# Kernel tuning notes

Hardware: AMD Instinct MI355X
Metric: run time of the kernel (lower is better)

## Reference

```python
import math
import jax, jax.numpy as jnp
import numpy as np

# --- module constants (from init_kwargs) ---
N_PIX = 1024
NV = 64
PIX_SCALE = 0.1            # arcsec / pixel
SIGMA_PIX = 0.8
TRUNCATE = 3.0
FOV_HALF = 0.5 * (N_PIX - 1) * PIX_SCALE


def setup_inputs() -> dict:
    key = jax.random.key(0)
    k1, k2, k3 = jax.random.split(key, 3)
    n_clouds, k_vel = 200_000, 8
    # positions uniform inside the field of view (slightly inset)
    pos_img = (jax.random.uniform(k1, (n_clouds, k_vel, 2), dtype=jnp.float32) * 2.0 - 1.0) * (FOV_HALF * 0.95)
    # uniform velocity axis and in-range cloud velocities
    vel_axis = (-400.0 + 12.5 * jnp.arange(NV, dtype=jnp.float32))
    vel_chan = jax.random.uniform(k2, (n_clouds, k_vel), dtype=jnp.float32) * 780.0 - 395.0
    flux = jax.random.uniform(k3, (n_clouds, k_vel), dtype=jnp.float32)
    # normalized separable Gaussian kernel, truncated at TRUNCATE sigma
    half = int(math.ceil(TRUNCATE * SIGMA_PIX))
    x = jnp.arange(-half, half + 1, dtype=jnp.float32)
    g1d = jnp.exp(-0.5 * (x / SIGMA_PIX) ** 2)
    g1d = g1d / g1d.sum()
    kernel2d = (g1d[:, None] * g1d[None, :])[None, None]  # (1,1,7,7)
    return {"pos_img": pos_img, "vel_chan": vel_chan, "flux": flux,
            "vel_axis": vel_axis, "kernel2d": kernel2d}


def reference(pos_img, vel_chan, flux, vel_axis, kernel2d):
    Nv = vel_axis.shape[0]
    vel0 = vel_axis[0]
    dv = vel_axis[1] - vel_axis[0]

    ra = pos_img[..., 0].reshape(-1)   # (M,)
    dec = pos_img[..., 1].reshape(-1)
    vel = vel_chan.reshape(-1)
    flx = flux.reshape(-1)

    # nearest (floor) voxel index per point; fractional parts are unused
    ix0 = jnp.floor((ra + FOV_HALF) / PIX_SCALE).astype(jnp.int32)
    iy0 = jnp.floor((dec + FOV_HALF) / PIX_SCALE).astype(jnp.int32)
    iv0 = jnp.floor((vel - vel0) / dv).astype(jnp.int32)

    margin = kernel2d.shape[-1] // 2 + 1
    mask = ((ix0 >= -margin) & (ix0 < N_PIX + margin)
            & (iy0 >= -margin) & (iy0 < N_PIX + margin)
            & (iv0 >= 0) & (iv0 < Nv))
    flx = jnp.where(mask, flx, 0.0)

    # scatter-add fluxes into flattened cube (out-of-range indices dropped)
    idx_flat = (iv0 * N_PIX + iy0) * N_PIX + ix0
    cube = (jnp.zeros(Nv * N_PIX * N_PIX, dtype=flx.dtype)
            .at[idx_flat].add(flx, mode="drop")
            .reshape(Nv, N_PIX, N_PIX))

    # 'same' 2D Gaussian convolution per velocity channel
    out = jax.lax.conv_general_dilated(cube[:, None, :, :], kernel2d,
                                       window_strides=(1, 1), padding="SAME")
    return out[:, 0]
```

## Files before the change

kernel.cpp:

```cpp
#include <hip/hip_runtime.h>
#include <math.h>

#define N_PIX 1024
#define NV 64
#define NT 16
#define TILE 64
#define HALO 70
#define CAP 320
#define NBINS (NV * NT * NT)
#define CUBE_ELEMS (NV * N_PIX * N_PIX)
#define RS 72
#define HS 68

__global__ __launch_bounds__(256) void splat_bin(
    const float2* __restrict__ pos,
    const float*  __restrict__ vel_chan,
    const float*  __restrict__ flux,
    const float*  __restrict__ vel_axis,
    unsigned*     __restrict__ cnt,
    uint2*        __restrict__ entries, int M)
{
    int i = blockIdx.x * 256 + threadIdx.x;
    if (i >= M) return;

    const float FOV_HALF = 51.15f;
    const float INV_PIX  = 10.0f;
    const float vel0 = vel_axis[0];
    const float dv   = vel_axis[1] - vel0;

    float2 p = pos[i];
    float  v = vel_chan[i];
    float  f = flux[i];

    int ix0 = (int)floorf((p.x + FOV_HALF) * INV_PIX);
    int iy0 = (int)floorf((p.y + FOV_HALF) * INV_PIX);
    int iv0 = (int)floorf((v - vel0) / dv);

    const int margin = 4;
    if (!(ix0 >= -margin && ix0 < N_PIX + margin &&
          iy0 >= -margin && iy0 < N_PIX + margin &&
          iv0 >= 0 && iv0 < NV)) return;

    int idx = (iv0 * N_PIX + iy0) * N_PIX + ix0;
    if (idx < 0 || idx >= CUBE_ELEMS) return;
    int iv = idx >> 20;
    int iy = (idx >> 10) & 1023;
    int ix = idx & 1023;

    int tx = ix >> 6, ty = iy >> 6;
    int fx = ix & 63, fy = iy & 63;

    #pragma unroll
    for (int dy = -1; dy <= 1; ++dy) {
        if (dy < 0 && (fy >= 3 || ty == 0)) continue;
        if (dy > 0 && (fy < 61 || ty == NT - 1)) continue;
        int ly  = fy + 3 - 64 * dy;
        int byb = (iv * NT + (ty + dy)) * NT;
        #pragma unroll
        for (int dx = -1; dx <= 1; ++dx) {
            if (dx < 0 && (fx >= 3 || tx == 0)) continue;
            if (dx > 0 && (fx < 61 || tx == NT - 1)) continue;
            int lx  = fx + 3 - 64 * dx;
            int bin = byb + tx + dx;
            unsigned pos_ = atomicAdd(&cnt[bin], 1u);
            if (pos_ < CAP)
                entries[(size_t)bin * CAP + pos_] =
                    make_uint2((unsigned)((ly << 7) | lx), __float_as_uint(f));
        }
    }
}

__global__ __launch_bounds__(256) void conv_tile(
    const unsigned* __restrict__ cnt,
    const uint2*    __restrict__ entries,
    const float*    __restrict__ k2d,
    float*          __restrict__ out)
{
    __shared__ float raw[HALO * RS];
    __shared__ float hb [HALO * HS];

    const int t   = threadIdx.x;
    const int ch  = blockIdx.y;
    const int bin = ch * (NT * NT) + blockIdx.x;

    float g[7];
    {
        float g3 = sqrtf(k2d[24]);
        #pragma unroll
        for (int j = 0; j < 7; ++j) g[j] = k2d[21 + j] / g3;
    }

    for (int i4 = t; i4 < HALO * RS / 4; i4 += 256)
        ((float4*)raw)[i4] = make_float4(0.f, 0.f, 0.f, 0.f);
    __syncthreads();

    unsigned n = cnt[bin];
    if (n > CAP) n = CAP;
    const uint2* e = entries + (size_t)bin * CAP;
    for (unsigned i = t; i < n; i += 256) {
        uint2 u = e[i];
        atomicAdd(&raw[(u.x >> 7) * RS + (u.x & 127)], __uint_as_float(u.y));
    }
    __syncthreads();

    for (int p = t; p < HALO * 16; p += 256) {
        int r  = p >> 4;
        int xg = (p & 15) << 2;
        const float* rp = &raw[r * RS + xg];
        float4 a = *(const float4*)(rp);
        float4 b = *(const float4*)(rp + 4);
        float4 c = *(const float4*)(rp + 8);
        float rr[12] = {a.x, a.y, a.z, a.w, b.x, b.y, b.z, b.w, c.x, c.y, c.z, c.w};
        float s0 = 0.f, s1 = 0.f, s2 = 0.f, s3 = 0.f;
        #pragma unroll
        for (int j = 0; j < 7; ++j) {
            s0 = fmaf(rr[j],     g[j], s0);
            s1 = fmaf(rr[j + 1], g[j], s1);
            s2 = fmaf(rr[j + 2], g[j], s2);
            s3 = fmaf(rr[j + 3], g[j], s3);
        }
        *(float4*)&hb[r * HS + xg] = make_float4(s0, s1, s2, s3);
    }
    __syncthreads();

    const int xg   = (t & 15) << 2;
    const int rblk = t >> 4;
    const int q0   = rblk * 4;

    float4 w[8];
    #pragma unroll
    for (int j = 0; j < 6; ++j)
        w[j] = *(const float4*)&hb[(q0 + j) * HS + xg];

    const int ty = blockIdx.x >> 4, tx = blockIdx.x & 15;
    float* __restrict__ dst = out + ((size_t)ch << 20);
    const int row0 = ty * TILE + q0;
    const int colb = tx * TILE + xg;

    #pragma unroll
    for (int i = 0; i < 4; ++i) {
        w[(i + 6) & 7] = *(const float4*)&hb[(q0 + i + 6) * HS + xg];
        float4 acc = make_float4(0.f, 0.f, 0.f, 0.f);
        #pragma unroll
        for (int k = 0; k < 7; ++k) {
            float4 h4 = w[(i + k) & 7];
            acc.x = fmaf(h4.x, g[k], acc.x);
            acc.y = fmaf(h4.y, g[k], acc.y);
            acc.z = fmaf(h4.z, g[k], acc.z);
            acc.w = fmaf(h4.w, g[k], acc.w);
        }
        *(float4*)(dst + ((size_t)(row0 + i) << 10) + colb) = acc;
    }
}

extern "C" void kernel_launch(void* const* d_in, const int* in_sizes, int n_in,
                              void* d_out, int out_size, void* d_ws, size_t ws_size,
                              hipStream_t stream)
{
    const float2* pos      = (const float2*)d_in[0];
    const float*  vel_chan = (const float*)d_in[1];
    const float*  flux     = (const float*)d_in[2];
    const float*  vel_axis = (const float*)d_in[3];
    const float*  k2d      = (const float*)d_in[4];
    float* out = (float*)d_out;

    unsigned* cnt     = (unsigned*)d_ws;
    uint2*    entries = (uint2*)((char*)d_ws + (1 << 20));

    const int M = in_sizes[1];

    hipMemsetAsync(cnt, 0, NBINS * sizeof(unsigned), stream);

    splat_bin<<<(M + 255) / 256, 256, 0, stream>>>(
        pos, vel_chan, flux, vel_axis, cnt, entries, M);

    conv_tile<<<dim3(NT * NT, NV), 256, 0, stream>>>(cnt, entries, k2d, out);
}
```

Before: 422.8 us.

## Fuse horizontal and vertical blur passes in registers; use nontemporal output stores

Each thread now computes the horizontal pass for the ten rows it needs directly into registers, then applies the vertical pass. This removes the intermediate shared-memory buffer and one barrier. The raw row stride changes to 76 floats, and the output is written with nontemporal stores so the large result cube streams past the cache. In exchange, horizontal work is recomputed (10 rows per 4 output rows instead of about 70/64), and register pressure goes up.

```diff
diff --git a/kernel.cpp b/kernel.cpp
--- a/kernel.cpp
+++ b/kernel.cpp
@@ -9,8 +9,9 @@
 #define CAP 320
 #define NBINS (NV * NT * NT)
 #define CUBE_ELEMS (NV * N_PIX * N_PIX)
-#define RS 72
-#define HS 68
+#define RS 76
+
+typedef float f32x4 __attribute__((ext_vector_type(4)));
 
 __global__ __launch_bounds__(256) void splat_bin(
     const float2* __restrict__ pos,
@@ -77,7 +78,6 @@
     float*          __restrict__ out)
 {
     __shared__ float raw[HALO * RS];
-    __shared__ float hb [HALO * HS];
 
     const int t   = threadIdx.x;
     const int ch  = blockIdx.y;
@@ -103,53 +103,43 @@
     }
     __syncthreads();
 
-    for (int p = t; p < HALO * 16; p += 256) {
-        int r  = p >> 4;
-        int xg = (p & 15) << 2;
-        const float* rp = &raw[r * RS + xg];
+    const int xg = (t & 15) << 2;
+    const int q0 = (t >> 4) << 2;
+
+    float4 h[10];
+    #pragma unroll
+    for (int j = 0; j < 10; ++j) {
+        const float* rp = &raw[(q0 + j) * RS + xg];
         float4 a = *(const float4*)(rp);
         float4 b = *(const float4*)(rp + 4);
         float4 c = *(const float4*)(rp + 8);
         float rr[12] = {a.x, a.y, a.z, a.w, b.x, b.y, b.z, b.w, c.x, c.y, c.z, c.w};
         float s0 = 0.f, s1 = 0.f, s2 = 0.f, s3 = 0.f;
         #pragma unroll
-        for (int j = 0; j < 7; ++j) {
-            s0 = fmaf(rr[j],     g[j], s0);
-            s1 = fmaf(rr[j + 1], g[j], s1);
-            s2 = fmaf(rr[j + 2], g[j], s2);
-            s3 = fmaf(rr[j + 3], g[j], s3);
+        for (int jj = 0; jj < 7; ++jj) {
+            s0 = fmaf(rr[jj],     g[jj], s0);
+            s1 = fmaf(rr[jj + 1], g[jj], s1);
+            s2 = fmaf(rr[jj + 2], g[jj], s2);
+            s3 = fmaf(rr[jj + 3], g[jj], s3);
         }
-        *(float4*)&hb[r * HS + xg] = make_float4(s0, s1, s2, s3);
+        h[j] = make_float4(s0, s1, s2, s3);
     }
-    __syncthreads();
-
-    const int xg   = (t & 15) << 2;
-    const int rblk = t >> 4;
-    const int q0   = rblk * 4;
-
-    float4 w[8];
-    #pragma unroll
-    for (int j = 0; j < 6; ++j)
-        w[j] = *(const float4*)&hb[(q0 + j) * HS + xg];
 
     const int ty = blockIdx.x >> 4, tx = blockIdx.x & 15;
-    float* __restrict__ dst = out + ((size_t)ch << 20);
-    const int row0 = ty * TILE + q0;
-    const int colb = tx * TILE + xg;
-
+    float* __restrict__ dst = out + ((size_t)ch << 20)
+                            + ((size_t)(ty * TILE + q0) << 10) + tx * TILE + xg;
     #pragma unroll
     for (int i = 0; i < 4; ++i) {
-        w[(i + 6) & 7] = *(const float4*)&hb[(q0 + i + 6) * HS + xg];
         float4 acc = make_float4(0.f, 0.f, 0.f, 0.f);
         #pragma unroll
         for (int k = 0; k < 7; ++k) {
-            float4 h4 = w[(i + k) & 7];
-            acc.x = fmaf(h4.x, g[k], acc.x);
-            acc.y = fmaf(h4.y, g[k], acc.y);
-            acc.z = fmaf(h4.z, g[k], acc.z);
-            acc.w = fmaf(h4.w, g[k], acc.w);
+            acc.x = fmaf(h[i + k].x, g[k], acc.x);
+            acc.y = fmaf(h[i + k].y, g[k], acc.y);
+            acc.z = fmaf(h[i + k].z, g[k], acc.z);
+            acc.w = fmaf(h[i + k].w, g[k], acc.w);
         }
-        *(float4*)(dst + ((size_t)(row0 + i) << 10) + colb) = acc;
+        f32x4 av; av.x = acc.x; av.y = acc.y; av.z = acc.z; av.w = acc.w;
+        __builtin_nontemporal_store(av, (f32x4*)(dst + ((size_t)i << 10)));
     }
 }
 
```

Result: slower. 452.1 us (+6.9%).
